# Optimization experiments

Measured on AMD Instinct MI355X. Metric: run time of the kernel, lower is better.

Reference implementation:

```python
import jax, jax.numpy as jnp
import numpy as np
from jax import lax


def binarize_weight(w):
    # per-output-channel scaling alpha = mean(|w|), binary weight = sign(w)*alpha
    alpha = jnp.mean(jnp.abs(w), axis=(1, 2, 3), keepdims=True)  # [O,1,1,1]
    wb = jnp.sign(w) * alpha
    # STE: forward uses wb, gradient passes straight through to w
    return w + lax.stop_gradient(wb - w)


def pixel_unshuffle2(x):
    # NCHW, factor 2: out[:, c*4 + i*2 + j] = x[:, c, i::2, j::2]
    B, C, H, W = x.shape
    x = x.reshape(B, C, H // 2, 2, W // 2, 2)
    x = x.transpose(0, 1, 3, 5, 2, 4)
    return x.reshape(B, C * 4, H // 2, W // 2)


def setup_inputs() -> dict:
    key = jax.random.key(0)
    ks = jax.random.split(key, 5)
    x = jax.random.normal(ks[0], (16, 256, 128, 128), dtype=jnp.float32)
    conv_w = jax.random.normal(ks[1], (128, 256, 3, 3), dtype=jnp.float32) * 0.05
    move1_b = jax.random.normal(ks[2], (128,), dtype=jnp.float32) * 0.01
    prelu_w = jax.random.uniform(ks[3], (128,), dtype=jnp.float32) * 0.25
    move2_b = jax.random.normal(ks[4], (128,), dtype=jnp.float32) * 0.01
    scale = jnp.ones((1,), dtype=jnp.float32)
    return {"x": x, "conv_w": conv_w, "move1_b": move1_b,
            "prelu_w": prelu_w, "move2_b": move2_b, "scale": scale}


def reference(x, conv_w, move1_b, prelu_w, move2_b, scale):
    wb = binarize_weight(conv_w)
    out = lax.conv_general_dilated(
        x, wb, window_strides=(1, 1), padding=((1, 1), (1, 1)),
        dimension_numbers=("NCHW", "OIHW", "NCHW"))  # [B,128,H,W]
    out = out + move1_b[None, :, None, None]
    a = prelu_w[None, :, None, None]
    out = jnp.where(out > 0, out, a * out)
    out = out + move2_b[None, :, None, None]
    shortcut = x[:, : x.shape[1] // 2, :, :] * scale[0]
    out = out + shortcut
    return pixel_unshuffle2(out)  # [B,512,H/2,W/2]
```

## Files before the change

kernel.cpp:

```cpp
#include <hip/hip_runtime.h>
#include <stdint.h>

typedef unsigned short ushort_t;
typedef __bf16 bf16x8 __attribute__((ext_vector_type(8)));
typedef float f32x4 __attribute__((ext_vector_type(4)));

#define NB   16
#define CIN  256
#define COUT 128
#define HH   128
#define WW   128
#define HP   130
#define WP   130
#define KTAP 9
#define KTOT 2304

__device__ __forceinline__ ushort_t f2bf(float f) {
  union { float f; uint32_t u; } v; v.f = f;
  uint32_t u = v.u;
  uint32_t r = (u + 0x7fffu + ((u >> 16) & 1u)) >> 16;
  return (ushort_t)r;
}
__device__ __forceinline__ float bf2f(ushort_t b) {
  union { uint32_t u; float f; } v; v.u = ((uint32_t)b) << 16;
  return v.f;
}
__device__ __forceinline__ void gload_lds16(const void* g, void* l) {
  __builtin_amdgcn_global_load_lds((const __attribute__((address_space(1))) void*)g,
                                   (__attribute__((address_space(3))) void*)l, 16, 0, 0);
}

__global__ void prep_w_kernel(const float* __restrict__ w,
                              ushort_t* __restrict__ sgnW,
                              float* __restrict__ alpha) {
  int o = blockIdx.x, c = threadIdx.x;
  const float* wo = w + (size_t)o * KTOT + c * 9;
  float s = 0.f;
#pragma unroll
  for (int tap = 0; tap < 9; ++tap) {
    float v = wo[tap];
    s += fabsf(v);
    ushort_t sg = (v > 0.f) ? 0x3F80 : (v < 0.f ? 0xBF80 : 0);
    sgnW[((size_t)tap * COUT + o) * CIN + c] = sg;
  }
  __shared__ float red[4];
  for (int off = 32; off; off >>= 1) s += __shfl_down(s, off, 64);
  if (!(c & 63)) red[c >> 6] = s;
  __syncthreads();
  if (!c) alpha[o] = (red[0] + red[1] + red[2] + red[3]) * (1.f / (float)KTOT);
}

__global__ void pad_kernel(ushort_t* __restrict__ xT) {
  int blk = blockIdx.x;
  int b = blk / 130, h = blk - b * 130;
  int t = threadIdx.x;
  uint32_t* row = (uint32_t*)(xT + ((size_t)b * HP + h) * WP * CIN);
  if (h == 0 || h == 129) {
    for (int i = t; i < WP * CIN / 2; i += 256) row[i] = 0;
  } else {
    if (t < 128) row[t] = 0;
    else         row[129 * (CIN / 2) + (t - 128)] = 0;
  }
}

__global__ void transpose_kernel(const float* __restrict__ x,
                                 ushort_t* __restrict__ xT) {
  int bid = blockIdx.x;
  int ct = bid & 3;
  int wt = (bid >> 2) & 1;
  int h  = (bid >> 3) & 127;
  int b  = bid >> 10;
  int c0 = ct * 64, w0 = wt * 64;
  __shared__ float tile[64][65];
  int t = threadIdx.x;
  const float* src = x + (((size_t)b * CIN + c0) * HH + h) * WW + w0;
#pragma unroll 4
  for (int it = 0; it < 16; ++it) {
    int cl = it * 4 + (t >> 6);
    tile[cl][t & 63] = src[(size_t)cl * (HH * WW) + (t & 63)];
  }
  __syncthreads();
  int cb = (t & 7) * 8;
  int wl = t >> 3;
#pragma unroll
  for (int wp = 0; wp < 2; ++wp) {
    int w = wp * 32 + wl;
    uint32_t pk[4];
#pragma unroll
    for (int j = 0; j < 4; ++j)
      pk[j] = (uint32_t)f2bf(tile[cb + 2 * j][w]) |
              ((uint32_t)f2bf(tile[cb + 2 * j + 1][w]) << 16);
    size_t idx = ((((size_t)b * HP + h + 1) * WP) + (w0 + w + 1)) * CIN + c0 + cb;
    *(uint4*)(xT + idx) = *(uint4*)pk;
  }
}

__global__ __launch_bounds__(256, 2) void conv_gemm(
    const ushort_t* __restrict__ xT, const ushort_t* __restrict__ sgnW,
    const float* __restrict__ alpha, const float* __restrict__ mv1,
    const float* __restrict__ pw, const float* __restrict__ mv2,
    const float* __restrict__ scale, float* __restrict__ out) {
  __shared__ __align__(16) ushort_t As[2][128 * 64];
  __shared__ __align__(16) ushort_t Bs[2][128 * 64];

  int bid = blockIdx.x;
  int wg = ((bid & 7) << 8) | (bid >> 3);
  int b = wg >> 7, h = wg & 127;

  int t = threadIdx.x, wv = t >> 6, l = t & 63;
  int wr = wv >> 1, wc = wv & 1;

  int crow = l >> 3;
  int se = (l & 7) ^ crow;
  int lg = l >> 4, rA = l & 15;

  f32x4 acc[4][4] = {};

  const ushort_t* xb = xT + ((size_t)b * HP + h) * WP * CIN;

#define STAGE(ksv, buf)                                                        \
  {                                                                            \
    int i0q_ = (ksv) / 9, tap_ = (ksv) - 9 * i0q_;                             \
    int kh_ = tap_ / 3, kw_ = tap_ - kh_ * 3;                                  \
    const ushort_t* gA_ = xb + (kh_ * WP + kw_) * CIN + (i0q_ << 6) + se * 8;  \
    const ushort_t* gB_ = sgnW + (size_t)tap_ * (COUT * CIN) + (i0q_ << 6) + se * 8; \
    _Pragma("unroll")                                                          \
    for (int q = 0; q < 4; ++q) {                                              \
      int c_ = wv * 4 + q;                                                     \
      int m_ = c_ * 8 + crow;                                                  \
      gload_lds16(gA_ + (size_t)m_ * CIN, (char*)&As[buf][0] + c_ * 1024);     \
      gload_lds16(gB_ + (size_t)m_ * CIN, (char*)&Bs[buf][0] + c_ * 1024);     \
    }                                                                          \
  }

  STAGE(0, 0);
  for (int ks = 0; ks < 36; ++ks) {
    int cur = ks & 1;
    if (ks < 35) {
      STAGE(ks + 1, cur ^ 1);
      asm volatile("s_waitcnt vmcnt(8)" ::: "memory");
    } else {
      asm volatile("s_waitcnt vmcnt(0)" ::: "memory");
    }
    __builtin_amdgcn_s_barrier();
    asm volatile("" ::: "memory");
    const char* Ab = (const char*)&As[0][0] + cur * (128 * 64 * 2);
    const char* Bb = (const char*)&Bs[0][0] + cur * (128 * 64 * 2);
#pragma unroll
    for (int kk = 0; kk < 2; ++kk) {
      bf16x8 av[4], bv[4];
#pragma unroll
      for (int mi = 0; mi < 4; ++mi) {
        int m = wr * 64 + mi * 16 + rA;
        int slot = (kk * 4 + lg) ^ (m & 7);
        av[mi] = *(const bf16x8*)(Ab + m * 128 + slot * 16);
      }
#pragma unroll
      for (int ni = 0; ni < 4; ++ni) {
        int o = wc * 64 + ni * 16 + rA;
        int slot = (kk * 4 + lg) ^ (o & 7);
        bv[ni] = *(const bf16x8*)(Bb + o * 128 + slot * 16);
      }
#pragma unroll
      for (int mi = 0; mi < 4; ++mi)
#pragma unroll
        for (int ni = 0; ni < 4; ++ni)
          acc[mi][ni] = __builtin_amdgcn_mfma_f32_16x16x32_bf16(av[mi], bv[ni], acc[mi][ni], 0, 0, 0);
    }
    __builtin_amdgcn_s_barrier();
    asm volatile("" ::: "memory");
  }

  float sc0 = scale[0];
  const ushort_t* scrow = xT + (((size_t)b * HP + h + 1) * WP + 1) * CIN;
  size_t outBase = (((size_t)b * 512 + (h & 1) * 2) * 64 + (h >> 1)) * 64;
#pragma unroll
  for (int ni = 0; ni < 4; ++ni) {
    int o = wc * 64 + ni * 16 + rA;
    float al = alpha[o], b1 = mv1[o], p = pw[o], b2 = mv2[o];
#pragma unroll
    for (int mi = 0; mi < 4; ++mi) {
#pragma unroll
      for (int r = 0; r < 4; ++r) {
        int w = wr * 64 + mi * 16 + lg * 4 + r;
        float v = acc[mi][ni][r] * al + b1;
        v = v > 0.f ? v : p * v;
        v += b2;
        v += bf2f(scrow[(size_t)w * CIN + o]) * sc0;
        out[outBase + (size_t)(o * 4 + (w & 1)) * 4096 + (w >> 1)] = v;
      }
    }
  }
}

extern "C" void kernel_launch(void* const* d_in, const int* in_sizes, int n_in,
                              void* d_out, int out_size, void* d_ws, size_t ws_size,
                              hipStream_t stream) {
  const float* x      = (const float*)d_in[0];
  const float* conv_w = (const float*)d_in[1];
  const float* mv1    = (const float*)d_in[2];
  const float* pw     = (const float*)d_in[3];
  const float* mv2    = (const float*)d_in[4];
  const float* scale  = (const float*)d_in[5];
  float* out = (float*)d_out;

  const size_t XT_ELEMS = (size_t)NB * HP * WP * CIN;
  ushort_t* xT   = (ushort_t*)d_ws;
  ushort_t* sgnW = xT + XT_ELEMS;
  float*    alpha = (float*)(sgnW + (size_t)KTAP * COUT * CIN);

  prep_w_kernel<<<COUT, 256, 0, stream>>>(conv_w, sgnW, alpha);
  pad_kernel<<<NB * HP, 256, 0, stream>>>(xT);
  transpose_kernel<<<NB * HH * 2 * 4, 256, 0, stream>>>(x, xT);
  conv_gemm<<<NB * HH, 256, 0, stream>>>(xT, sgnW, alpha, mv1, pw, mv2, scale, out);
}
```

Measured before the change: 673.2 us.

## Drop LDS double buffering in conv GEMM and raise occupancy to four blocks

Replaces the two-stage LDS double-buffered pipeline with a single buffer loaded and consumed between two __syncthreads per k-step. The loop is restructured as 4 channel chunks by 9 unrolled taps, and launch bounds are raised to 4 blocks per CU. Halving LDS use and constraining registers is meant to let more workgroups hide latency through occupancy instead of explicit prefetch. The cost is that global loads no longer overlap MFMA work within a block, and register pressure for the 64 accumulators per lane may cause spills.

```diff
diff --git a/kernel.cpp b/kernel.cpp
--- a/kernel.cpp
+++ b/kernel.cpp
@@ -95,13 +95,13 @@
   }
 }
 
-__global__ __launch_bounds__(256, 2) void conv_gemm(
+__global__ __launch_bounds__(256, 4) void conv_gemm(
     const ushort_t* __restrict__ xT, const ushort_t* __restrict__ sgnW,
     const float* __restrict__ alpha, const float* __restrict__ mv1,
     const float* __restrict__ pw, const float* __restrict__ mv2,
     const float* __restrict__ scale, float* __restrict__ out) {
-  __shared__ __align__(16) ushort_t As[2][128 * 64];
-  __shared__ __align__(16) ushort_t Bs[2][128 * 64];
+  __shared__ __align__(16) ushort_t As[128 * 64];
+  __shared__ __align__(16) ushort_t Bs[128 * 64];
 
   int bid = blockIdx.x;
   int wg = ((bid & 7) << 8) | (bid >> 3);
@@ -118,57 +118,43 @@
 
   const ushort_t* xb = xT + ((size_t)b * HP + h) * WP * CIN;
 
-#define STAGE(ksv, buf)                                                        \
-  {                                                                            \
-    int i0q_ = (ksv) / 9, tap_ = (ksv) - 9 * i0q_;                             \
-    int kh_ = tap_ / 3, kw_ = tap_ - kh_ * 3;                                  \
-    const ushort_t* gA_ = xb + (kh_ * WP + kw_) * CIN + (i0q_ << 6) + se * 8;  \
-    const ushort_t* gB_ = sgnW + (size_t)tap_ * (COUT * CIN) + (i0q_ << 6) + se * 8; \
-    _Pragma("unroll")                                                          \
-    for (int q = 0; q < 4; ++q) {                                              \
-      int c_ = wv * 4 + q;                                                     \
-      int m_ = c_ * 8 + crow;                                                  \
-      gload_lds16(gA_ + (size_t)m_ * CIN, (char*)&As[buf][0] + c_ * 1024);     \
-      gload_lds16(gB_ + (size_t)m_ * CIN, (char*)&Bs[buf][0] + c_ * 1024);     \
-    }                                                                          \
-  }
-
-  STAGE(0, 0);
-  for (int ks = 0; ks < 36; ++ks) {
-    int cur = ks & 1;
-    if (ks < 35) {
-      STAGE(ks + 1, cur ^ 1);
-      asm volatile("s_waitcnt vmcnt(8)" ::: "memory");
-    } else {
-      asm volatile("s_waitcnt vmcnt(0)" ::: "memory");
+  for (int i0q = 0; i0q < 4; ++i0q) {
+#pragma unroll
+    for (int tap = 0; tap < 9; ++tap) {
+      const int kh = tap / 3, kw = tap - kh * 3;
+      __syncthreads();
+      const ushort_t* gA = xb + (kh * WP + kw) * CIN + (i0q << 6) + se * 8;
+      const ushort_t* gB = sgnW + (size_t)tap * (COUT * CIN) + (i0q << 6) + se * 8;
+#pragma unroll
+      for (int q = 0; q < 4; ++q) {
+        int c = wv * 4 + q;
+        int m = c * 8 + crow;
+        gload_lds16(gA + (size_t)m * CIN, (char*)As + c * 1024);
+        gload_lds16(gB + (size_t)m * CIN, (char*)Bs + c * 1024);
+      }
+      __syncthreads();
+#pragma unroll
+      for (int kk = 0; kk < 2; ++kk) {
+        bf16x8 av[4], bv[4];
+#pragma unroll
+        for (int mi = 0; mi < 4; ++mi) {
+          int m = wr * 64 + mi * 16 + rA;
+          int slot = (kk * 4 + lg) ^ (m & 7);
+          av[mi] = *(const bf16x8*)((const char*)As + m * 128 + slot * 16);
+        }
+#pragma unroll
+        for (int ni = 0; ni < 4; ++ni) {
+          int o = wc * 64 + ni * 16 + rA;
+          int slot = (kk * 4 + lg) ^ (o & 7);
+          bv[ni] = *(const bf16x8*)((const char*)Bs + o * 128 + slot * 16);
+        }
+#pragma unroll
+        for (int mi = 0; mi < 4; ++mi)
+#pragma unroll
+          for (int ni = 0; ni < 4; ++ni)
+            acc[mi][ni] = __builtin_amdgcn_mfma_f32_16x16x32_bf16(av[mi], bv[ni], acc[mi][ni], 0, 0, 0);
+      }
     }
-    __builtin_amdgcn_s_barrier();
-    asm volatile("" ::: "memory");
-    const char* Ab = (const char*)&As[0][0] + cur * (128 * 64 * 2);
-    const char* Bb = (const char*)&Bs[0][0] + cur * (128 * 64 * 2);
-#pragma unroll
-    for (int kk = 0; kk < 2; ++kk) {
-      bf16x8 av[4], bv[4];
-#pragma unroll
-      for (int mi = 0; mi < 4; ++mi) {
-        int m = wr * 64 + mi * 16 + rA;
-        int slot = (kk * 4 + lg) ^ (m & 7);
-        av[mi] = *(const bf16x8*)(Ab + m * 128 + slot * 16);
-      }
-#pragma unroll
-      for (int ni = 0; ni < 4; ++ni) {
-        int o = wc * 64 + ni * 16 + rA;
-        int slot = (kk * 4 + lg) ^ (o & 7);
-        bv[ni] = *(const bf16x8*)(Bb + o * 128 + slot * 16);
-      }
-#pragma unroll
-      for (int mi = 0; mi < 4; ++mi)
-#pragma unroll
-        for (int ni = 0; ni < 4; ++ni)
-          acc[mi][ni] = __builtin_amdgcn_mfma_f32_16x16x32_bf16(av[mi], bv[ni], acc[mi][ni], 0, 0, 0);
-    }
-    __builtin_amdgcn_s_barrier();
-    asm volatile("" ::: "memory");
   }
 
   float sc0 = scale[0];
```

New measurement: 679.8 us. No clear change (+1.0%).
